# Kernel tuning notes

Measured on AMD Instinct MI355X. Metric: run time of the kernel, lower is better.

Reference implementation:

```python
import jax, jax.numpy as jnp
import numpy as np

BB, T, N, M, P = 512, 128, 32, 16, 16
Q_SCALE, R_SCALE = 0.08, 0.3


def _mT(x):
    return jnp.swapaxes(x, -1, -2)


def setup_inputs() -> dict:
    key = jax.random.key(0)
    k = jax.random.split(key, 6)
    Y = jax.random.normal(k[0], (BB, T, P), dtype=jnp.float32)
    U = jax.random.normal(k[1], (BB, T, M), dtype=jnp.float32)
    # stable transition matrix (spectral radius < 1) so the filter doesn't blow up over T steps
    A = 0.8 * jnp.eye(N, dtype=jnp.float32) + 0.05 * jax.random.normal(k[2], (N, N), dtype=jnp.float32)
    Bmat = 0.1 * jax.random.normal(k[3], (N, M), dtype=jnp.float32)
    Cmat = jax.random.normal(k[4], (P, N), dtype=jnp.float32) / jnp.sqrt(jnp.float32(N))
    mu0 = jax.random.normal(k[5], (N,), dtype=jnp.float32)
    Sigma0 = jnp.eye(N, dtype=jnp.float32)
    Q = (Q_SCALE ** 2) * jnp.eye(N, dtype=jnp.float32)
    R = (R_SCALE ** 2) * jnp.eye(P, dtype=jnp.float32)
    return dict(Y=Y, U=U, A=A, Bmat=Bmat, Cmat=Cmat, mu0=mu0, Sigma0=Sigma0, Q=Q, R=R)


def _kalman_smooth(Y, U, A, Bm, C, mu0, Sigma0, Q, R):
    Bb, Tt, _ = Y.shape
    n = A.shape[0]
    I = jnp.eye(n, dtype=Y.dtype)
    Yt = jnp.swapaxes(Y, 0, 1)  # [T,B,p]
    Ut = jnp.swapaxes(U, 0, 1)  # [T,B,m]

    def fstep(carry, yu):
        mu, Sig = carry  # [B,n], [B,n,n]
        y, u = yu
        mu_p = mu @ A.T + u @ Bm.T                       # predicted mean  [B,n]
        Sig_p = A @ Sig @ A.T + Q                        # predicted cov   [B,n,n]
        r = y - mu_p @ C.T                               # innovation      [B,p]
        S = C @ Sig_p @ C.T + R                          # innovation cov  [B,p,p]
        S = 0.5 * (S + _mT(S))
        PCT = Sig_p @ C.T                                # [B,n,p]
        K = _mT(jnp.linalg.solve(S, _mT(PCT)))           # Kalman gain     [B,n,p]
        mu_f = mu_p + jnp.einsum('bnp,bp->bn', K, r)
        IKC = I - K @ C
        Sig_f = IKC @ Sig_p @ _mT(IKC) + K @ R @ _mT(K)  # Joseph form
        Sig_f = 0.5 * (Sig_f + _mT(Sig_f))
        return (mu_f, Sig_f), (mu_f, Sig_f, mu_p, Sig_p)

    mu_init = jnp.broadcast_to(mu0, (Bb, n))
    Sig_init = jnp.broadcast_to(Sigma0, (Bb, n, n))
    _, (mus_f, Sigs_f, mus_p, Sigs_p) = jax.lax.scan(fstep, (mu_init, Sig_init), (Yt, Ut))

    # RTS smoother (backward recursion via reverse scan)
    def sstep(carry, xs):
        mu_T, Sig_T = carry  # smoothed at t+1
        Sig_f, Sig_p, mu_f, mu_p = xs  # filtered at t, predicted at t+1
        J = _mT(jnp.linalg.solve(_mT(Sig_p), _mT(Sig_f @ A.T)))  # [B,n,n]
        mu_s = mu_f + jnp.einsum('bij,bj->bi', J, mu_T - mu_p)
        Sig_s = Sig_f + J @ (Sig_T - Sig_p) @ _mT(J)
        Sig_s = 0.5 * (Sig_s + _mT(Sig_s))
        return (mu_s, Sig_s), (mu_s, Sig_s)

    xs = (Sigs_f[:-1], Sigs_p[1:], mus_f[:-1], mus_p[1:])
    carry0 = (mus_f[-1], Sigs_f[-1])
    _, (mus_s, Sigs_s) = jax.lax.scan(sstep, carry0, xs, reverse=True)
    mus_s = jnp.concatenate([mus_s, mus_f[-1:]], axis=0)      # [T,B,n]
    Sigs_s = jnp.concatenate([Sigs_s, Sigs_f[-1:]], axis=0)   # [T,B,n,n]
    return jnp.swapaxes(mus_s, 0, 1), jnp.swapaxes(Sigs_s, 0, 1)


def reference(Y, U, A, Bmat, Cmat, mu0, Sigma0, Q, R):
    return _kalman_smooth(Y, U, A, Bmat, Cmat, mu0, Sigma0, Q, R)
```

## Files before the change

kernel.cpp:

```cpp
#include <hip/hip_runtime.h>

constexpr int BB = 512, T = 128, N = 32, M = 16, P = 16;
constexpr int NP = N * P;
constexpr int NN = N * N;
constexpr int NM = N * M;

typedef float f4 __attribute__((ext_vector_type(4)));

__device__ __forceinline__ void bar_lds() {
    asm volatile("s_waitcnt lgkmcnt(0)" ::: "memory");
    __builtin_amdgcn_s_barrier();
    asm volatile("" ::: "memory");
}

__device__ __forceinline__ void load_row32(const float* __restrict__ src, float* dst) {
    const float4* s4 = reinterpret_cast<const float4*>(src);
    #pragma unroll
    for (int c = 0; c < 8; ++c) {
        float4 v = s4[c];
        dst[4*c+0] = v.x; dst[4*c+1] = v.y; dst[4*c+2] = v.z; dst[4*c+3] = v.w;
    }
}
__device__ __forceinline__ void load_row16(const float* __restrict__ src, float* dst) {
    const float4* s4 = reinterpret_cast<const float4*>(src);
    #pragma unroll
    for (int c = 0; c < 4; ++c) {
        float4 v = s4[c];
        dst[4*c+0] = v.x; dst[4*c+1] = v.y; dst[4*c+2] = v.z; dst[4*c+3] = v.w;
    }
}

__global__ __launch_bounds__(256) void k_fwd(
    const float* __restrict__ A, const float* __restrict__ C,
    const float* __restrict__ Q, const float* __restrict__ R,
    const float* __restrict__ Sigma0,
    float* __restrict__ K_all, float* __restrict__ Sp_all, float* __restrict__ Sf_all,
    int* __restrict__ tconv_out)
{
    __shared__ float A_l[N][N + 1], C_l[P][N + 1], Q_l[N][N + 1], R_l[P][P + 1];
    __shared__ float Sig[N][N + 1], Tmp[N][N + 1], Sp[N][N + 1], CP[P][N + 1];
    __shared__ float Aug[P][49];
    __shared__ float red[4];
    const int tid = threadIdx.x;
    const int i0 = tid >> 5, j = tid & 31;
    const int pD = tid >> 4, q = tid & 15;
    const float TOL = 1e-4f;

    for (int idx = tid; idx < NN; idx += 256) {
        A_l[idx >> 5][idx & 31] = A[idx];
        Q_l[idx >> 5][idx & 31] = Q[idx];
        Sig[idx >> 5][idx & 31] = Sigma0[idx];
    }
    for (int idx = tid; idx < P * N; idx += 256) C_l[idx >> 5][idx & 31] = C[idx];
    for (int idx = tid; idx < P * P; idx += 256) R_l[idx >> 4][idx & 15] = R[idx];
    bar_lds();

    float Arow[4][32], Cq[32], Qjv[4];
    #pragma unroll
    for (int e = 0; e < 4; ++e) {
        #pragma unroll
        for (int k = 0; k < 32; ++k) Arow[e][k] = A_l[i0 + 8*e][k];
        Qjv[e] = Q_l[j][i0 + 8*e];
    }
    #pragma unroll
    for (int k = 0; k < 32; ++k) Cq[k] = C_l[q][k];
    const float Rv = R_l[pD][q];

    float prevSig[4];
    #pragma unroll
    for (int e = 0; e < 4; ++e) prevSig[e] = Sig[i0 + 8*e][j];

    int t_conv = T;

    for (int t = 0; t < T; ++t) {
        {
            float sc[32];
            #pragma unroll
            for (int k = 0; k < 32; ++k) sc[k] = Sig[k][j];
            #pragma unroll
            for (int e = 0; e < 4; ++e) {
                float s = 0.f;
                #pragma unroll
                for (int k = 0; k < 32; ++k) s += Arow[e][k] * sc[k];
                Tmp[i0 + 8*e][j] = s;
            }
        }
        bar_lds();
        {
            float tr[32];
            #pragma unroll
            for (int k = 0; k < 32; ++k) tr[k] = Tmp[j][k];
            #pragma unroll
            for (int e = 0; e < 4; ++e) {
                const int c = i0 + 8*e;
                float s = Qjv[e];
                #pragma unroll
                for (int k = 0; k < 32; ++k) s += tr[k] * Arow[e][k];
                Sp[j][c] = s;
                Sp_all[t * NN + tid + 256*e] = s;
            }
        }
        bar_lds();
        {
            float spc[32];
            #pragma unroll
            for (int k = 0; k < 32; ++k) spc[k] = Sp[k][j];
            #pragma unroll
            for (int e = 0; e < 2; ++e) {
                const int p = i0 + 8*e;
                float s = 0.f;
                #pragma unroll
                for (int k = 0; k < 32; ++k) s += C_l[p][k] * spc[k];
                CP[p][j] = s;
            }
        }
        bar_lds();
        {
            float cpr[32];
            #pragma unroll
            for (int k = 0; k < 32; ++k) cpr[k] = CP[pD][k];
            float s = Rv;
            #pragma unroll
            for (int k = 0; k < 32; ++k) s += cpr[k] * Cq[k];
            Aug[pD][q] = s;
        }
        #pragma unroll
        for (int e = 0; e < 2; ++e) {
            const int p = i0 + 8*e;
            Aug[p][16 + j] = CP[p][j];
        }
        bar_lds();
        if (tid < 64) {
            const int r = tid >> 2, qd = tid & 3;
            float a[12];
            #pragma unroll
            for (int c = 0; c < 12; ++c) a[c] = Aug[r][qd * 12 + c];
            #pragma unroll
            for (int p = 0; p < P; ++p) {
                const int pq = p / 12;
                const int lp = p - 12 * pq;
                const float pivv = __shfl(a[lp], (p << 2) + pq);
                const float f    = __shfl(a[lp], (tid & ~3) + pq);
                const float pinv = 1.0f / pivv;
                const float fp = f * pinv;
                float pr[12];
                #pragma unroll
                for (int c = 0; c < 12; ++c) pr[c] = __shfl(a[c], (p << 2) + qd);
                #pragma unroll
                for (int c = 0; c < 12; ++c)
                    a[c] = (r == p) ? pr[c] * pinv : a[c] - fp * pr[c];
            }
            if (qd) {
                #pragma unroll
                for (int c = 0; c < 12; ++c) Aug[r][qd * 12 + c] = a[c];
            }
        }
        bar_lds();
        #pragma unroll
        for (int e = 0; e < 2; ++e) {
            const int idx = tid + 256*e;
            K_all[t * NP + idx] = Aug[idx & 15][16 + (idx >> 4)];
        }
        float wmax = 0.f;
        {
            float cpj[16];
            #pragma unroll
            for (int p = 0; p < 16; ++p) cpj[p] = CP[p][j];
            #pragma unroll
            for (int e = 0; e < 4; ++e) {
                const int i = i0 + 8*e;
                float s = Sp[i][j];
                #pragma unroll
                for (int p = 0; p < 16; ++p) s -= Aug[p][16 + i] * cpj[p];
                Sig[i][j] = s;
                Sf_all[t * NN + tid + 256*e] = s;
                wmax = fmaxf(wmax, fabsf(s - prevSig[e]));
                prevSig[e] = s;
            }
        }
        #pragma unroll
        for (int m = 1; m < 64; m <<= 1)
            wmax = fmaxf(wmax, __shfl_xor(wmax, m));
        if ((tid & 63) == 0) red[tid >> 6] = wmax;
        bar_lds();
        const float g = fmaxf(fmaxf(red[0], red[1]), fmaxf(red[2], red[3]));
        if (g <= TOL && t < T - 1) { t_conv = t; break; }
    }

    if (t_conv < T - 1) {
        float kv[2], spv[4], sfv[4];
        #pragma unroll
        for (int e = 0; e < 2; ++e) {
            const int idx = tid + 256*e;
            kv[e] = Aug[idx & 15][16 + (idx >> 4)];
        }
        #pragma unroll
        for (int e = 0; e < 4; ++e) {
            spv[e] = Sp[i0 + 8*e][j];
            sfv[e] = Sig[i0 + 8*e][j];
        }
        for (int s = t_conv + 1; s < T; ++s) {
            #pragma unroll
            for (int e = 0; e < 2; ++e) K_all[s * NP + tid + 256*e] = kv[e];
            #pragma unroll
            for (int e = 0; e < 4; ++e) {
                Sp_all[s * NN + tid + 256*e] = spv[e];
                Sf_all[s * NN + tid + 256*e] = sfv[e];
            }
        }
    }
    if (tid == 0) *tconv_out = t_conv;
}

__global__ __launch_bounds__(256) void k_jhm(
    const float* __restrict__ A, const float* __restrict__ C, const float* __restrict__ Bm,
    const float* __restrict__ Sp_all, const float* __restrict__ Sf_all,
    const float* __restrict__ K_all,
    float* __restrict__ J_all, float* __restrict__ H_all,
    float* __restrict__ G_all, float* __restrict__ D_all,
    float* __restrict__ E_all, float* __restrict__ F_all)
{
    const int t = blockIdx.x;
    __shared__ float A_l[N][N + 1], Sf[N][N + 1], Sp1[N][N + 1];
    __shared__ float Aug[N][65], W[N][N + 1], Jl[N][N + 1];
    __shared__ float C_l[P][N + 1], B_l[N][M + 1], Kl[N][P + 1];
    const int tid = threadIdx.x;
    const bool hasJ = (t < T - 1);

    for (int idx = tid; idx < NN; idx += 256) A_l[idx >> 5][idx & 31] = A[idx];
    for (int idx = tid; idx < P * N; idx += 256) C_l[idx >> 5][idx & 31] = C[idx];
    for (int idx = tid; idx < NM; idx += 256) B_l[idx >> 4][idx & 15] = Bm[idx];
    for (int idx = tid; idx < NP; idx += 256) Kl[idx >> 4][idx & 15] = K_all[t * NP + idx];
    if (hasJ) {
        for (int idx = tid; idx < NN; idx += 256) {
            Sf[idx >> 5][idx & 31]  = Sf_all[t * NN + idx];
            Sp1[idx >> 5][idx & 31] = Sp_all[(t + 1) * NN + idx];
        }
    }
    __syncthreads();

    if (hasJ) {
        #pragma unroll
        for (int e = 0; e < 4; ++e) {
            int idx = tid + e * 256; int i = idx >> 5, j = idx & 31;
            float s = 0.f;
            #pragma unroll
            for (int k = 0; k < N; ++k) s += A_l[i][k] * Sf[k][j];
            Aug[i][32 + j] = s;
            Aug[i][j] = Sp1[i][j];
        }
        __syncthreads();
        {
            int r = tid >> 3, c0 = (tid & 7) * 8;
            for (int p = 0; p < N; ++p) {
                float pinv = 1.0f / Aug[p][p];
                float f = Aug[r][p];
                float prow[8], mine[8];
                #pragma unroll
                for (int c = 0; c < 8; ++c) { prow[c] = Aug[p][c0 + c]; mine[c] = Aug[r][c0 + c]; }
                __syncthreads();
                float fp = f * pinv;
                #pragma unroll
                for (int c = 0; c < 8; ++c)
                    Aug[r][c0 + c] = (r == p) ? prow[c] * pinv : mine[c] - fp * prow[c];
                __syncthreads();
            }
        }
        #pragma unroll
        for (int e = 0; e < 4; ++e) {
            int idx = tid + e * 256; int i = idx >> 5, j = idx & 31;
            float v = Aug[j][32 + i];
            Jl[i][j] = v;
            J_all[t * NN + idx] = v;
        }
        __syncthreads();
        #pragma unroll
        for (int e = 0; e < 4; ++e) {
            int idx = tid + e * 256; int i = idx >> 5, j = idx & 31;
            float s = 0.f;
            #pragma unroll
            for (int k = 0; k < N; ++k) s += Jl[i][k] * Sp1[k][j];
            W[i][j] = s;
        }
        __syncthreads();
        #pragma unroll
        for (int e = 0; e < 4; ++e) {
            int idx = tid + e * 256; int i = idx >> 5, j = idx & 31;
            float s = Sf[i][j];
            #pragma unroll
            for (int k = 0; k < N; ++k) s -= W[i][k] * Jl[j][k];
            H_all[t * NN + idx] = s;
        }
    }
    __syncthreads();
    #pragma unroll
    for (int e = 0; e < 4; ++e) {
        int idx = tid + e * 256; int i = idx >> 5, j = idx & 31;
        float s = 0.f;
        #pragma unroll
        for (int p = 0; p < P; ++p) s += Kl[i][p] * C_l[p][j];
        W[i][j] = s;
    }
    __syncthreads();
    #pragma unroll
    for (int e = 0; e < 4; ++e) {
        int idx = tid + e * 256; int i = idx >> 5, j = idx & 31;
        float s = A_l[i][j];
        #pragma unroll
        for (int k = 0; k < N; ++k) s -= W[i][k] * A_l[k][j];
        G_all[t * NN + idx] = s;
    }
    #pragma unroll
    for (int e = 0; e < 2; ++e) {
        int idx = tid + e * 256; int i = idx >> 4, m = idx & 15;
        float s = B_l[i][m];
        #pragma unroll
        for (int k = 0; k < N; ++k) s -= W[i][k] * B_l[k][m];
        D_all[t * NM + idx] = s;
    }
    if (hasJ) {
        #pragma unroll
        for (int e = 0; e < 4; ++e) {
            int idx = tid + e * 256; int i = idx >> 5, j = idx & 31;
            float s = (i == j) ? 1.f : 0.f;
            #pragma unroll
            for (int k = 0; k < N; ++k) s -= Jl[i][k] * A_l[k][j];
            E_all[t * NN + idx] = s;
        }
        #pragma unroll
        for (int e = 0; e < 2; ++e) {
            int idx = tid + e * 256; int i = idx >> 4, m = idx & 15;
            float s = 0.f;
            #pragma unroll
            for (int k = 0; k < N; ++k) s += Jl[i][k] * B_l[k][m];
            F_all[t * NM + idx] = s;
        }
    }
}

__global__ __launch_bounds__(256) void k_sscan(
    const float* __restrict__ Sf_all,
    const float* __restrict__ J_all, const float* __restrict__ H_all,
    float* __restrict__ Ss_all, const int* __restrict__ tconv_ptr)
{
    __shared__ float Ss[N][N + 1], W[N][N + 1], Hl[N][N + 1];
    __shared__ float red[4];
    const int tid = threadIdx.x;
    const int i0 = tid >> 5, j = tid & 31;
    const int t_conv = *tconv_ptr;
    const float TOL = 1e-3f;

    for (int idx = tid; idx < NN; idx += 256) {
        float v = Sf_all[(size_t)(T - 1) * NN + idx];
        Ss[idx >> 5][idx & 31] = v;
        Ss_all[(size_t)(T - 1) * NN + idx] = v;
    }
    bar_lds();
    float prevSs[4];
    #pragma unroll
    for (int e = 0; e < 4; ++e) prevSs[e] = Ss[j][i0 + 8*e];

    for (int t = T - 2; t >= 0; --t) {
        float jr[4][32];
        #pragma unroll
        for (int e = 0; e < 4; ++e)
            load_row32(J_all + (size_t)t * NN + (i0 + 8*e) * 32, jr[e]);
        #pragma unroll
        for (int e = 0; e < 4; ++e)
            Hl[i0 + 8*e][j] = H_all[(size_t)t * NN + tid + 256*e];
        {
            float sc[32];
            #pragma unroll
            for (int k = 0; k < 32; ++k) sc[k] = Ss[k][j];
            #pragma unroll
            for (int e = 0; e < 4; ++e) {
                float s = 0.f;
                #pragma unroll
                for (int k = 0; k < 32; ++k) s += jr[e][k] * sc[k];
                W[i0 + 8*e][j] = s;
            }
        }
        bar_lds();
        float localmax = 0.f;
        {
            float wr[32];
            #pragma unroll
            for (int k = 0; k < 32; ++k) wr[k] = W[j][k];
            #pragma unroll
            for (int e = 0; e < 4; ++e) {
                const int c = i0 + 8*e;
                float s = Hl[j][c];
                #pragma unroll
                for (int k = 0; k < 32; ++k) s += wr[k] * jr[e][k];
                Ss[j][c] = s;
                Ss_all[(size_t)t * NN + tid + 256*e] = s;
                localmax = fmaxf(localmax, fabsf(s - prevSs[e]));
                prevSs[e] = s;
            }
        }
        #pragma unroll
        for (int m = 1; m < 64; m <<= 1)
            localmax = fmaxf(localmax, __shfl_xor(localmax, m));
        if ((tid & 63) == 0) red[tid >> 6] = localmax;
        bar_lds();
        const float g = fmaxf(fmaxf(red[0], red[1]), fmaxf(red[2], red[3]));
        if (g <= TOL && (t - 1 >= t_conv)) {
            for (int s = t_conv; s <= t - 1; ++s) {
                #pragma unroll
                for (int e = 0; e < 4; ++e)
                    Ss_all[(size_t)s * NN + tid + 256*e] = prevSs[e];
            }
            t = t_conv;
        }
    }
}

__global__ __launch_bounds__(64, 1) void k_mu(
    const float* __restrict__ Y, const float* __restrict__ U,
    const float* __restrict__ mu0,
    const float* __restrict__ K_all, const float* __restrict__ J_all,
    const float* __restrict__ G_all, const float* __restrict__ D_all,
    const float* __restrict__ E_all, const float* __restrict__ F_all,
    const int* __restrict__ tconv_ptr,
    float* __restrict__ out_mus)
{
    const int b = blockIdx.x;
    const int lane = threadIdx.x;
    const int j = lane & 31;
    const int half = lane >> 5;
    __shared__ float mfh[T][N];
    __shared__ float cfh[T][N];
    const int t_conv = *tconv_ptr;
    const float* Yb = Y + (size_t)b * T * P;
    const float* Ub = U + (size_t)b * T * M;

    for (int it = 0; it < T / 2; ++it) {
        const int t = it * 2 + half;
        float dr[16], kr[16], uu[16], yy[16];
        load_row16(D_all + t * NM + j * 16, dr);
        load_row16(K_all + t * NP + j * 16, kr);
        load_row16(Ub + t * M, uu);
        load_row16(Yb + t * P, yy);
        float s0 = 0.f, s1 = 0.f, s2 = 0.f, s3 = 0.f;
        #pragma unroll
        for (int m = 0; m < 16; m += 4) {
            s0 += dr[m+0]*uu[m+0]; s1 += dr[m+1]*uu[m+1];
            s2 += dr[m+2]*uu[m+2]; s3 += dr[m+3]*uu[m+3];
            s0 += kr[m+0]*yy[m+0]; s1 += kr[m+1]*yy[m+1];
            s2 += kr[m+2]*yy[m+2]; s3 += kr[m+3]*yy[m+3];
        }
        cfh[t][j] = (s0 + s1) + (s2 + s3);
    }
    __syncthreads();

    float mu = mu0[j];
    float gr[32];
    load_row32(G_all + j * 32, gr);
    const int tv = (t_conv < T - 1) ? t_conv : (T - 1);
    float cn = cfh[0][j];
    int t = 0;
    for (; t < tv; ++t) {
        float grn[32];
        load_row32(G_all + (size_t)(t + 1) * NN + j * 32, grn);
        const float cnn = cfh[t + 1][j];
        float s0 = 0.f, s1 = 0.f, s2 = 0.f, s3 = 0.f;
        #pragma unroll
        for (int k = 0; k < 32; k += 4) {
            s0 += gr[k+0] * __shfl(mu, k+0);
            s1 += gr[k+1] * __shfl(mu, k+1);
            s2 += gr[k+2] * __shfl(mu, k+2);
            s3 += gr[k+3] * __shfl(mu, k+3);
        }
        mu = ((s0 + s1) + (s2 + s3)) + cn;
        if (lane < 32) mfh[t][j] = mu;
        #pragma unroll
        for (int c = 0; c < 32; ++c) gr[c] = grn[c];
        cn = cnn;
    }
    for (; t < T; ++t) {
        const float cnn = (t + 1 < T) ? cfh[t + 1][j] : 0.f;
        float s0 = 0.f, s1 = 0.f, s2 = 0.f, s3 = 0.f;
        #pragma unroll
        for (int k = 0; k < 32; k += 4) {
            s0 += gr[k+0] * __shfl(mu, k+0);
            s1 += gr[k+1] * __shfl(mu, k+1);
            s2 += gr[k+2] * __shfl(mu, k+2);
            s3 += gr[k+3] * __shfl(mu, k+3);
        }
        mu = ((s0 + s1) + (s2 + s3)) + cn;
        if (lane < 32) mfh[t][j] = mu;
        cn = cnn;
    }
    if (lane < 32) out_mus[((size_t)b * T + (T - 1)) * N + j] = mu;
    __syncthreads();

    for (int it = 0; it < T / 2; ++it) {
        const int tt = it * 2 + half;
        if (tt < T - 1) {
            float er[32], fr[16], uu[16];
            load_row32(E_all + (size_t)tt * NN + j * 32, er);
            load_row16(F_all + tt * NM + j * 16, fr);
            load_row16(Ub + (tt + 1) * M, uu);
            float s0 = 0.f, s1 = 0.f, s2 = 0.f, s3 = 0.f;
            #pragma unroll
            for (int k = 0; k < 32; k += 4) {
                s0 += er[k+0] * mfh[tt][k+0];
                s1 += er[k+1] * mfh[tt][k+1];
                s2 += er[k+2] * mfh[tt][k+2];
                s3 += er[k+3] * mfh[tt][k+3];
            }
            #pragma unroll
            for (int m = 0; m < 16; m += 4) {
                s0 -= fr[m+0]*uu[m+0]; s1 -= fr[m+1]*uu[m+1];
                s2 -= fr[m+2]*uu[m+2]; s3 -= fr[m+3]*uu[m+3];
            }
            cfh[tt][j] = (s0 + s1) + (s2 + s3);
        }
    }
    __syncthreads();

    float ms = mu;
    const int tp = (t_conv < T - 2) ? t_conv : (T - 2);
    float jr[32];
    load_row32(J_all + (size_t)tp * NN + j * 32, jr);
    float cb = cfh[T - 2][j];
    for (t = T - 2; t >= tp; --t) {
        const float cbn = (t - 1 >= 0) ? cfh[t - 1][j] : 0.f;
        float s0 = 0.f, s1 = 0.f, s2 = 0.f, s3 = 0.f;
        #pragma unroll
        for (int k = 0; k < 32; k += 4) {
            s0 += jr[k+0] * __shfl(ms, k+0);
            s1 += jr[k+1] * __shfl(ms, k+1);
            s2 += jr[k+2] * __shfl(ms, k+2);
            s3 += jr[k+3] * __shfl(ms, k+3);
        }
        ms = ((s0 + s1) + (s2 + s3)) + cb;
        if (lane < 32) out_mus[((size_t)b * T + t) * N + j] = ms;
        cb = cbn;
    }
    if (t >= 0) {
        load_row32(J_all + (size_t)t * NN + j * 32, jr);
        for (; t >= 0; --t) {
            float jrn[32];
            #pragma unroll
            for (int c = 0; c < 32; ++c) jrn[c] = 0.f;
            if (t > 0) load_row32(J_all + (size_t)(t - 1) * NN + j * 32, jrn);
            const float cbn = (t - 1 >= 0) ? cfh[t - 1][j] : 0.f;
            float s0 = 0.f, s1 = 0.f, s2 = 0.f, s3 = 0.f;
            #pragma unroll
            for (int k = 0; k < 32; k += 4) {
                s0 += jr[k+0] * __shfl(ms, k+0);
                s1 += jr[k+1] * __shfl(ms, k+1);
                s2 += jr[k+2] * __shfl(ms, k+2);
                s3 += jr[k+3] * __shfl(ms, k+3);
            }
            ms = ((s0 + s1) + (s2 + s3)) + cb;
            if (lane < 32) out_mus[((size_t)b * T + t) * N + j] = ms;
            cb = cbn;
            #pragma unroll
            for (int c = 0; c < 32; ++c) jr[c] = jrn[c];
        }
    }
}

__global__ __launch_bounds__(256) void k_bcast(
    const float* __restrict__ Ss_all, f4* __restrict__ out4)
{
    const f4* src = (const f4*)Ss_all;
    const long long total = (long long)BB * T * (NN / 4);
    const long long stride = (long long)gridDim.x * blockDim.x;
    for (long long g = blockIdx.x * (long long)blockDim.x + threadIdx.x; g < total; g += stride) {
        int e4 = (int)(g & 255);
        long long bt = g >> 8;
        int t = (int)(bt & (T - 1));
        __builtin_nontemporal_store(src[t * 256 + e4], &out4[g]);
    }
}

extern "C" void kernel_launch(void* const* d_in, const int* in_sizes, int n_in,
                              void* d_out, int out_size, void* d_ws, size_t ws_size,
                              hipStream_t stream)
{
    (void)in_sizes; (void)n_in; (void)out_size; (void)ws_size;
    const float* Y      = (const float*)d_in[0];
    const float* U      = (const float*)d_in[1];
    const float* A      = (const float*)d_in[2];
    const float* Bm     = (const float*)d_in[3];
    const float* C      = (const float*)d_in[4];
    const float* mu0    = (const float*)d_in[5];
    const float* Sigma0 = (const float*)d_in[6];
    const float* Q      = (const float*)d_in[7];
    const float* R      = (const float*)d_in[8];

    float* ws     = (float*)d_ws;
    float* K_all  = ws;
    float* Sp_all = K_all + T * NP;
    float* Sf_all = Sp_all + T * NN;
    float* J_all  = Sf_all + T * NN;
    float* H_all  = J_all + T * NN;
    float* Ss_all = H_all + T * NN;
    float* G_all  = Ss_all + T * NN;
    float* D_all  = G_all + T * NN;
    float* E_all  = D_all + T * NM;
    float* F_all  = E_all + T * NN;
    int*   tconv  = (int*)(F_all + T * NM);

    float* out_mus  = (float*)d_out;
    float* out_sigs = out_mus + (size_t)BB * T * N;

    hipLaunchKernelGGL(k_fwd,   dim3(1),    dim3(256), 0, stream, A, C, Q, R, Sigma0, K_all, Sp_all, Sf_all, tconv);
    hipLaunchKernelGGL(k_jhm,   dim3(T),    dim3(256), 0, stream, A, C, Bm, Sp_all, Sf_all, K_all, J_all, H_all, G_all, D_all, E_all, F_all);
    hipLaunchKernelGGL(k_sscan, dim3(1),    dim3(256), 0, stream, Sf_all, J_all, H_all, Ss_all, tconv);
    hipLaunchKernelGGL(k_mu,    dim3(BB),   dim3(64),  0, stream, Y, U, mu0, K_all, J_all, G_all, D_all, E_all, F_all, tconv, out_mus);
    hipLaunchKernelGGL(k_bcast, dim3(4096), dim3(256), 0, stream, Ss_all, (f4*)out_sigs);
}
```

Before: 568.7 us.

## Halve serial mean recursions by pairing consecutive steps into two-step transition products

Adds a kernel that precomputes products of consecutive transition matrices (G[t+1]G[t] and J[t-1]J[t]). The per-batch forward filter and backward smoother mean recursions then advance two timesteps per serial iteration. The skipped intermediate steps are filled in afterwards with parallel matrix-vector passes. This roughly halves the serial dependency chain of shuffle-based matvecs, at the cost of an extra launch, extra workspace, and additional parallel fill-in work.

```diff
diff --git a/kernel.cpp b/kernel.cpp
--- a/kernel.cpp
+++ b/kernel.cpp
@@ -338,6 +338,46 @@
     }
 }
 
+__global__ __launch_bounds__(256) void k_pair(
+    const float* __restrict__ G_all, const float* __restrict__ J_all,
+    float* __restrict__ G2_all, float* __restrict__ JJ_all)
+{
+    const int pt = blockIdx.x;
+    const int tid = threadIdx.x;
+    const int t = 2 * pt;
+    __shared__ float Ma[N][N + 1], Mb[N][N + 1];
+
+    for (int idx = tid; idx < NN; idx += 256) {
+        Ma[idx >> 5][idx & 31] = G_all[(size_t)(t + 1) * NN + idx];
+        Mb[idx >> 5][idx & 31] = G_all[(size_t)t * NN + idx];
+    }
+    __syncthreads();
+    #pragma unroll
+    for (int e = 0; e < 4; ++e) {
+        int idx = tid + e * 256; int i = idx >> 5, jj = idx & 31;
+        float s = 0.f;
+        #pragma unroll
+        for (int k = 0; k < N; ++k) s += Ma[i][k] * Mb[k][jj];
+        G2_all[(size_t)pt * NN + idx] = s;
+    }
+    if (pt >= 1) {
+        __syncthreads();
+        for (int idx = tid; idx < NN; idx += 256) {
+            Ma[idx >> 5][idx & 31] = J_all[(size_t)(t - 1) * NN + idx];
+            Mb[idx >> 5][idx & 31] = J_all[(size_t)t * NN + idx];
+        }
+        __syncthreads();
+        #pragma unroll
+        for (int e = 0; e < 4; ++e) {
+            int idx = tid + e * 256; int i = idx >> 5, jj = idx & 31;
+            float s = 0.f;
+            #pragma unroll
+            for (int k = 0; k < N; ++k) s += Ma[i][k] * Mb[k][jj];
+            JJ_all[(size_t)pt * NN + idx] = s;
+        }
+    }
+}
+
 __global__ __launch_bounds__(256) void k_sscan(
     const float* __restrict__ Sf_all,
     const float* __restrict__ J_all, const float* __restrict__ H_all,
@@ -421,6 +461,7 @@
     const float* __restrict__ K_all, const float* __restrict__ J_all,
     const float* __restrict__ G_all, const float* __restrict__ D_all,
     const float* __restrict__ E_all, const float* __restrict__ F_all,
+    const float* __restrict__ G2_all, const float* __restrict__ JJ_all,
     const int* __restrict__ tconv_ptr,
     float* __restrict__ out_mus)
 {
@@ -430,6 +471,7 @@
     const int half = lane >> 5;
     __shared__ float mfh[T][N];
     __shared__ float cfh[T][N];
+    __shared__ float c2h[T / 2][N];
     const int t_conv = *tconv_ptr;
     const float* Yb = Y + (size_t)b * T * P;
     const float* Ub = U + (size_t)b * T * M;
@@ -453,16 +495,36 @@
     }
     __syncthreads();
 
+    for (int it = 0; it < 32; ++it) {
+        const int pt = it * 2 + half;
+        const int t = pt * 2;
+        float grow[32];
+        load_row32(G_all + (size_t)(t + 1) * NN + j * 32, grow);
+        float s0 = 0.f, s1 = 0.f, s2 = 0.f, s3 = 0.f;
+        #pragma unroll
+        for (int k = 0; k < 32; k += 4) {
+            s0 += grow[k+0] * cfh[t][k+0];
+            s1 += grow[k+1] * cfh[t][k+1];
+            s2 += grow[k+2] * cfh[t][k+2];
+            s3 += grow[k+3] * cfh[t][k+3];
+        }
+        c2h[pt][j] = ((s0 + s1) + (s2 + s3)) + cfh[t + 1][j];
+    }
+    __syncthreads();
+
     float mu = mu0[j];
+    const int ptv0 = (t_conv + 1) >> 1;
+    const int ptv = (ptv0 < 64) ? ptv0 : 64;
     float gr[32];
-    load_row32(G_all + j * 32, gr);
-    const int tv = (t_conv < T - 1) ? t_conv : (T - 1);
-    float cn = cfh[0][j];
-    int t = 0;
-    for (; t < tv; ++t) {
+    load_row32(G2_all + j * 32, gr);
+    float cn = c2h[0][j];
+    int pt = 0;
+    for (; pt < ptv; ++pt) {
         float grn[32];
-        load_row32(G_all + (size_t)(t + 1) * NN + j * 32, grn);
-        const float cnn = cfh[t + 1][j];
+        #pragma unroll
+        for (int c = 0; c < 32; ++c) grn[c] = 0.f;
+        if (pt + 1 < 64) load_row32(G2_all + (size_t)(pt + 1) * NN + j * 32, grn);
+        const float cnn = (pt + 1 < 64) ? c2h[pt + 1][j] : 0.f;
         float s0 = 0.f, s1 = 0.f, s2 = 0.f, s3 = 0.f;
         #pragma unroll
         for (int k = 0; k < 32; k += 4) {
@@ -472,13 +534,13 @@
             s3 += gr[k+3] * __shfl(mu, k+3);
         }
         mu = ((s0 + s1) + (s2 + s3)) + cn;
-        if (lane < 32) mfh[t][j] = mu;
+        if (lane < 32) mfh[2 * pt + 1][j] = mu;
         #pragma unroll
         for (int c = 0; c < 32; ++c) gr[c] = grn[c];
         cn = cnn;
     }
-    for (; t < T; ++t) {
-        const float cnn = (t + 1 < T) ? cfh[t + 1][j] : 0.f;
+    for (; pt < 64; ++pt) {
+        const float cnn = (pt + 1 < 64) ? c2h[pt + 1][j] : 0.f;
         float s0 = 0.f, s1 = 0.f, s2 = 0.f, s3 = 0.f;
         #pragma unroll
         for (int k = 0; k < 32; k += 4) {
@@ -488,10 +550,37 @@
             s3 += gr[k+3] * __shfl(mu, k+3);
         }
         mu = ((s0 + s1) + (s2 + s3)) + cn;
-        if (lane < 32) mfh[t][j] = mu;
+        if (lane < 32) mfh[2 * pt + 1][j] = mu;
         cn = cnn;
     }
     if (lane < 32) out_mus[((size_t)b * T + (T - 1)) * N + j] = mu;
+    __syncthreads();
+
+    for (int it = 0; it < 32; ++it) {
+        const int pt2 = it * 2 + half;
+        const int t = pt2 * 2;
+        float grow[32];
+        load_row32(G_all + (size_t)t * NN + j * 32, grow);
+        float s0 = 0.f, s1 = 0.f, s2 = 0.f, s3 = 0.f;
+        if (t == 0) {
+            #pragma unroll
+            for (int k = 0; k < 32; k += 4) {
+                s0 += grow[k+0] * mu0[k+0];
+                s1 += grow[k+1] * mu0[k+1];
+                s2 += grow[k+2] * mu0[k+2];
+                s3 += grow[k+3] * mu0[k+3];
+            }
+        } else {
+            #pragma unroll
+            for (int k = 0; k < 32; k += 4) {
+                s0 += grow[k+0] * mfh[t-1][k+0];
+                s1 += grow[k+1] * mfh[t-1][k+1];
+                s2 += grow[k+2] * mfh[t-1][k+2];
+                s3 += grow[k+3] * mfh[t-1][k+3];
+            }
+        }
+        mfh[t][j] = ((s0 + s1) + (s2 + s3)) + cfh[t][j];
+    }
     __syncthreads();
 
     for (int it = 0; it < T / 2; ++it) {
@@ -519,33 +608,34 @@
     }
     __syncthreads();
 
+    for (int it = 0; it < 32; ++it) {
+        const int pt2 = it * 2 + half + 1;
+        if (pt2 < 64) {
+            const int t = pt2 * 2;
+            float jrow[32];
+            load_row32(J_all + (size_t)(t - 1) * NN + j * 32, jrow);
+            float s0 = 0.f, s1 = 0.f, s2 = 0.f, s3 = 0.f;
+            #pragma unroll
+            for (int k = 0; k < 32; k += 4) {
+                s0 += jrow[k+0] * cfh[t][k+0];
+                s1 += jrow[k+1] * cfh[t][k+1];
+                s2 += jrow[k+2] * cfh[t][k+2];
+                s3 += jrow[k+3] * cfh[t][k+3];
+            }
+            c2h[pt2][j] = ((s0 + s1) + (s2 + s3)) + cfh[t - 1][j];
+        }
+    }
+    __syncthreads();
+
     float ms = mu;
-    const int tp = (t_conv < T - 2) ? t_conv : (T - 2);
+    const int tplmin = t_conv + 1;
+    int t = 126;
     float jr[32];
-    load_row32(J_all + (size_t)tp * NN + j * 32, jr);
-    float cb = cfh[T - 2][j];
-    for (t = T - 2; t >= tp; --t) {
-        const float cbn = (t - 1 >= 0) ? cfh[t - 1][j] : 0.f;
-        float s0 = 0.f, s1 = 0.f, s2 = 0.f, s3 = 0.f;
-        #pragma unroll
-        for (int k = 0; k < 32; k += 4) {
-            s0 += jr[k+0] * __shfl(ms, k+0);
-            s1 += jr[k+1] * __shfl(ms, k+1);
-            s2 += jr[k+2] * __shfl(ms, k+2);
-            s3 += jr[k+3] * __shfl(ms, k+3);
-        }
-        ms = ((s0 + s1) + (s2 + s3)) + cb;
-        if (lane < 32) out_mus[((size_t)b * T + t) * N + j] = ms;
-        cb = cbn;
-    }
-    if (t >= 0) {
-        load_row32(J_all + (size_t)t * NN + j * 32, jr);
-        for (; t >= 0; --t) {
-            float jrn[32];
-            #pragma unroll
-            for (int c = 0; c < 32; ++c) jrn[c] = 0.f;
-            if (t > 0) load_row32(J_all + (size_t)(t - 1) * NN + j * 32, jrn);
-            const float cbn = (t - 1 >= 0) ? cfh[t - 1][j] : 0.f;
+    float cb = c2h[63][j];
+    if (t >= tplmin) {
+        load_row32(JJ_all + (size_t)(t >> 1) * NN + j * 32, jr);
+        for (; t >= 2 && t >= tplmin; t -= 2) {
+            const float cbn = (t - 2 >= 2) ? c2h[(t - 2) >> 1][j] : 0.f;
             float s0 = 0.f, s1 = 0.f, s2 = 0.f, s3 = 0.f;
             #pragma unroll
             for (int k = 0; k < 32; k += 4) {
@@ -555,10 +645,70 @@
                 s3 += jr[k+3] * __shfl(ms, k+3);
             }
             ms = ((s0 + s1) + (s2 + s3)) + cb;
-            if (lane < 32) out_mus[((size_t)b * T + t) * N + j] = ms;
+            if (lane < 32) {
+                out_mus[((size_t)b * T + (t - 1)) * N + j] = ms;
+                mfh[t - 1][j] = ms;
+            }
             cb = cbn;
+        }
+    }
+    if (t >= 2) {
+        load_row32(JJ_all + (size_t)(t >> 1) * NN + j * 32, jr);
+        for (; t >= 2; t -= 2) {
+            float jrn[32];
+            #pragma unroll
+            for (int c = 0; c < 32; ++c) jrn[c] = 0.f;
+            if (t - 2 >= 2) load_row32(JJ_all + (size_t)((t - 2) >> 1) * NN + j * 32, jrn);
+            const float cbn = (t - 2 >= 2) ? c2h[(t - 2) >> 1][j] : 0.f;
+            float s0 = 0.f, s1 = 0.f, s2 = 0.f, s3 = 0.f;
+            #pragma unroll
+            for (int k = 0; k < 32; k += 4) {
+                s0 += jr[k+0] * __shfl(ms, k+0);
+                s1 += jr[k+1] * __shfl(ms, k+1);
+                s2 += jr[k+2] * __shfl(ms, k+2);
+                s3 += jr[k+3] * __shfl(ms, k+3);
+            }
+            ms = ((s0 + s1) + (s2 + s3)) + cb;
+            if (lane < 32) {
+                out_mus[((size_t)b * T + (t - 1)) * N + j] = ms;
+                mfh[t - 1][j] = ms;
+            }
+            cb = cbn;
             #pragma unroll
             for (int c = 0; c < 32; ++c) jr[c] = jrn[c];
+        }
+    }
+    {
+        float jrow[32];
+        load_row32(J_all + j * 32, jrow);
+        float s0 = 0.f, s1 = 0.f, s2 = 0.f, s3 = 0.f;
+        #pragma unroll
+        for (int k = 0; k < 32; k += 4) {
+            s0 += jrow[k+0] * __shfl(ms, k+0);
+            s1 += jrow[k+1] * __shfl(ms, k+1);
+            s2 += jrow[k+2] * __shfl(ms, k+2);
+            s3 += jrow[k+3] * __shfl(ms, k+3);
+        }
+        const float ms0 = ((s0 + s1) + (s2 + s3)) + cfh[0][j];
+        if (lane < 32) out_mus[(size_t)b * T * N + j] = ms0;
+    }
+    __syncthreads();
+
+    for (int it = 0; it < 32; ++it) {
+        const int pt2 = it * 2 + half + 1;
+        if (pt2 < 64) {
+            const int t2 = pt2 * 2;
+            float jrow[32];
+            load_row32(J_all + (size_t)t2 * NN + j * 32, jrow);
+            float s0 = 0.f, s1 = 0.f, s2 = 0.f, s3 = 0.f;
+            #pragma unroll
+            for (int k = 0; k < 32; k += 4) {
+                s0 += jrow[k+0] * mfh[t2+1][k+0];
+                s1 += jrow[k+1] * mfh[t2+1][k+1];
+                s2 += jrow[k+2] * mfh[t2+1][k+2];
+                s3 += jrow[k+3] * mfh[t2+1][k+3];
+            }
+            out_mus[((size_t)b * T + t2) * N + j] = ((s0 + s1) + (s2 + s3)) + cfh[t2][j];
         }
     }
 }
@@ -603,14 +753,17 @@
     float* D_all  = G_all + T * NN;
     float* E_all  = D_all + T * NM;
     float* F_all  = E_all + T * NN;
-    int*   tconv  = (int*)(F_all + T * NM);
+    float* G2_all = F_all + T * NM;
+    float* JJ_all = G2_all + (T / 2) * NN;
+    int*   tconv  = (int*)(JJ_all + (T / 2) * NN);
 
     float* out_mus  = (float*)d_out;
     float* out_sigs = out_mus + (size_t)BB * T * N;
 
-    hipLaunchKernelGGL(k_fwd,   dim3(1),    dim3(256), 0, stream, A, C, Q, R, Sigma0, K_all, Sp_all, Sf_all, tconv);
-    hipLaunchKernelGGL(k_jhm,   dim3(T),    dim3(256), 0, stream, A, C, Bm, Sp_all, Sf_all, K_all, J_all, H_all, G_all, D_all, E_all, F_all);
-    hipLaunchKernelGGL(k_sscan, dim3(1),    dim3(256), 0, stream, Sf_all, J_all, H_all, Ss_all, tconv);
-    hipLaunchKernelGGL(k_mu,    dim3(BB),   dim3(64),  0, stream, Y, U, mu0, K_all, J_all, G_all, D_all, E_all, F_all, tconv, out_mus);
-    hipLaunchKernelGGL(k_bcast, dim3(4096), dim3(256), 0, stream, Ss_all, (f4*)out_sigs);
-}
+    hipLaunchKernelGGL(k_fwd,   dim3(1),     dim3(256), 0, stream, A, C, Q, R, Sigma0, K_all, Sp_all, Sf_all, tconv);
+    hipLaunchKernelGGL(k_jhm,   dim3(T),     dim3(256), 0, stream, A, C, Bm, Sp_all, Sf_all, K_all, J_all, H_all, G_all, D_all, E_all, F_all);
+    hipLaunchKernelGGL(k_pair,  dim3(T / 2), dim3(256), 0, stream, G_all, J_all, G2_all, JJ_all);
+    hipLaunchKernelGGL(k_sscan, dim3(1),     dim3(256), 0, stream, Sf_all, J_all, H_all, Ss_all, tconv);
+    hipLaunchKernelGGL(k_mu,    dim3(BB),    dim3(64),  0, stream, Y, U, mu0, K_all, J_all, G_all, D_all, E_all, F_all, G2_all, JJ_all, tconv, out_mus);
+    hipLaunchKernelGGL(k_bcast, dim3(4096),  dim3(256), 0, stream, Ss_all, (f4*)out_sigs);
+}
```

After: 604.5 us. 6.3% more time.
